# Performance work log

Hardware: AMD Instinct MI355X
Metric: run time of the kernel (lower is better)

## Reference

```python
import jax, jax.numpy as jnp
import numpy as np

P = 16; D = 256; NH = 8; L = 4; E = 8; K = 2; B = 32; IMG = 224; NC = 1000; FF = 4 * D
N = (IMG // P) ** 2  # 196 patches
HD = D // NH  # head dim
EPS = 1e-5


def setup_inputs():
    key = jax.random.key(0)
    ks = iter(jax.random.split(key, 16))
    s = 0.02  # init scale keeps softmax/logits well-conditioned
    rn = lambda shape: jax.random.normal(next(ks), shape, jnp.float32) * s
    return dict(
        x=jax.random.normal(next(ks), (B, 3, IMG, IMG), jnp.float32),
        patch_w=rn((3 * P * P, D)), patch_b=jnp.zeros((D,), jnp.float32),
        cls_token=rn((1, 1, D)), pos_embed=rn((1, N + 1, D)),
        router_w=rn((L, D, E)), router_b=jnp.zeros((L, E), jnp.float32),
        ln1_g=jnp.ones((L, E, D), jnp.float32), ln1_b=jnp.zeros((L, E, D), jnp.float32),
        qkv_w=rn((L, E, D, 3 * D)), qkv_b=jnp.zeros((L, E, 3 * D), jnp.float32),
        proj_w=rn((L, E, D, D)), proj_b=jnp.zeros((L, E, D), jnp.float32),
        ln2_g=jnp.ones((L, E, D), jnp.float32), ln2_b=jnp.zeros((L, E, D), jnp.float32),
        fc1_w=rn((L, E, D, FF)), fc1_b=jnp.zeros((L, E, FF), jnp.float32),
        fc2_w=rn((L, E, FF, D)), fc2_b=jnp.zeros((L, E, D), jnp.float32),
        norm_g=jnp.ones((D,), jnp.float32), norm_b=jnp.zeros((D,), jnp.float32),
        head_w=rn((D, NC)), head_b=jnp.zeros((NC,), jnp.float32),
    )


def _ln(x, g, b):
    m = x.mean(-1, keepdims=True)
    v = ((x - m) ** 2).mean(-1, keepdims=True)
    return (x - m) * jax.lax.rsqrt(v + EPS) * g + b


def _block(x, g1, b1, wqkv, bqkv, wp, bp, g2, b2, w1, bias1, w2, bias2):
    # standard ViT block: LN -> MHA -> residual, LN -> MLP(GELU) -> residual
    bsz, S, _ = x.shape
    h = _ln(x, g1, b1)
    qkv = (h @ wqkv + bqkv).reshape(bsz, S, 3, NH, HD)
    q, k, v = qkv[:, :, 0], qkv[:, :, 1], qkv[:, :, 2]  # [B,S,NH,HD]
    scores = jnp.einsum('bqhd,bkhd->bhqk', q, k) / np.float32(np.sqrt(HD))
    attn = jax.nn.softmax(scores, axis=-1)
    o = jnp.einsum('bhqk,bkhd->bqhd', attn, v).reshape(bsz, S, D)
    x = x + o @ wp + bp
    h2 = _ln(x, g2, b2)
    x = x + jax.nn.gelu(h2 @ w1 + bias1, approximate=False) @ w2 + bias2
    return x


def _moe_layer(x, rw, rb, g1, b1, wqkv, bqkv, wp, bp, g2, b2, w1, bias1, w2, bias2):
    probs = jax.nn.softmax(x @ rw + rb, axis=-1)            # [B,S,E]
    topv, topi = jax.lax.top_k(probs, K)                    # [B,S,K]
    topv = topv / topv.sum(-1, keepdims=True)
    # dense all-expert compute (faithful to source), vmapped over experts
    eo = jax.vmap(_block, in_axes=(None,) + (0,) * 12)(
        x, g1, b1, wqkv, bqkv, wp, bp, g2, b2, w1, bias1, w2, bias2)  # [E,B,S,D]
    eo = jnp.moveaxis(eo, 0, 2)                             # [B,S,E,D]
    sel = jnp.take_along_axis(eo, topi[..., None], axis=2)  # [B,S,K,D]
    return (sel * topv[..., None]).sum(axis=2)


def reference(x, patch_w, patch_b, cls_token, pos_embed, router_w, router_b,
              ln1_g, ln1_b, qkv_w, qkv_b, proj_w, proj_b, ln2_g, ln2_b,
              fc1_w, fc1_b, fc2_w, fc2_b, norm_g, norm_b, head_w, head_b):
    bsz = x.shape[0]
    g = IMG // P
    # patch embed: stride==kernel conv == patch extraction + matmul
    patches = x.reshape(bsz, 3, g, P, g, P).transpose(0, 2, 4, 1, 3, 5).reshape(bsz, N, 3 * P * P)
    h = patches @ patch_w + patch_b                          # [B,N,D]
    cls = jnp.broadcast_to(cls_token, (bsz, 1, D))
    h = jnp.concatenate([cls, h], axis=1) + pos_embed        # [B,N+1,D]
    for l in range(L):
        h = _moe_layer(h, router_w[l], router_b[l], ln1_g[l], ln1_b[l],
                       qkv_w[l], qkv_b[l], proj_w[l], proj_b[l], ln2_g[l], ln2_b[l],
                       fc1_w[l], fc1_b[l], fc2_w[l], fc2_b[l])
    h = _ln(h, norm_g, norm_b)
    return h[:, 0] @ head_w + head_b                         # [B,NC]
```

## Files before the change

### kernel.cpp

```cpp
#include <hip/hip_runtime.h>
#include <math.h>

#define SEQ 197
#define BATCH 32
#define DIM 256
#define NHEAD 8
#define HDIM 32
#define NEXP 8
#define NLAYER 4
#define FFDIM 1024
#define NCLS 1000
#define NPATCH 196
#define TOK (BATCH * SEQ)
#define CAP 13120
#define YB 99
#define YB128 50
#define KT 64

__device__ __forceinline__ void gload16(const float* g, float* l) {
  __builtin_amdgcn_global_load_lds(
      (const __attribute__((address_space(1))) void*)g,
      (__attribute__((address_space(3))) void*)l, 16, 0, 0);
}

__global__ __launch_bounds__(256) void k_im2col(const float* __restrict__ x,
                                                float* __restrict__ Apat) {
  int idx = blockIdx.x * 256 + threadIdx.x;
  if (idx >= BATCH * NPATCH * 768) return;
  int cpp = idx % 768;
  int m = idx / 768;
  int n = m % NPATCH;
  int b = m / NPATCH;
  int c = cpp >> 8;
  int py = (cpp >> 4) & 15;
  int px = cpp & 15;
  int gy = n / 14, gx = n % 14;
  Apat[idx] = x[(((size_t)b * 3 + c) * 224 + gy * 16 + py) * 224 + gx * 16 + px];
}

__global__ __launch_bounds__(256) void k_foldw(const float* __restrict__ qw,
                                               const float* __restrict__ g1,
                                               float* __restrict__ w4) {
  size_t idx = (size_t)blockIdx.x * 256 + threadIdx.x;
  if (idx >= (size_t)32 * 256 * 768) return;
  size_t kn = idx % (256 * 768);
  int le = (int)(idx / (256 * 768));
  int k = (int)(kn / 768);
  w4[idx] = qw[idx] * g1[le * 256 + k];
}

__global__ __launch_bounds__(256) void k_foldb(const float* __restrict__ qw,
                                               const float* __restrict__ qb,
                                               const float* __restrict__ b1,
                                               float* __restrict__ b4) {
  int le = blockIdx.y;
  int col = blockIdx.x * 256 + threadIdx.x;
  const float* w = qw + (size_t)le * 256 * 768 + col;
  const float* lb = b1 + (size_t)le * 256;
  float acc = 0.f;
  for (int k = 0; k < 256; ++k) acc = fmaf(lb[k], w[(size_t)k * 768], acc);
  b4[(size_t)le * 768 + col] = acc + qb[(size_t)le * 768 + col];
}

__global__ __launch_bounds__(256) void k_gemm_t(
    const float* __restrict__ A, const float* __restrict__ W,
    const float* __restrict__ bias, const float* __restrict__ R,
    const float* __restrict__ X2, const float* __restrict__ PW,
    const int* __restrict__ ptok, const int* __restrict__ off_e,
    const int* __restrict__ cnt_e, float* __restrict__ out, int M, int N,
    int K, int Wld, int wcol, int bstride, int ebase, int mode, int flags) {
  __shared__ float As[2][16][68];
  __shared__ float Bs[2][16][128];
  int gx = gridDim.x, gy = gridDim.y;
  int nwg = gx * gy * gridDim.z;
  int lin = blockIdx.x + gx * (blockIdx.y + gy * blockIdx.z);
  int q8 = nwg >> 3, r8 = nwg & 7;
  int xcd = lin & 7, jj0 = lin >> 3;
  int nlin = (xcd < r8 ? xcd * (q8 + 1) : r8 * (q8 + 1) + (xcd - r8) * q8) + jj0;
  int bx = nlin % gx;
  int t1 = nlin / gx;
  int by = t1 % gy;
  int bz = t1 / gy;

  int e = ebase + bz;
  bool seg = (flags & 1) != 0;
  int rows = seg ? cnt_e[e] : M;
  int row0 = by * 64;
  if (row0 >= rows) return;
  int col0 = bx * 128;
  int tid = threadIdx.x;
  int base = seg ? off_e[e] : 0;
  const float* Wp = W + (size_t)e * K * Wld + wcol;
  const float* bp = bias + (size_t)e * bstride + wcol;

  int rr = tid >> 2, kq = (tid & 3) * 4;
  int r = row0 + rr;
  bool val = r < rows;
  int rc = val ? r : rows - 1;
  int gr0 = base + rc;
  int arow = seg ? ((flags & 2) ? ptok[gr0] : gr0) : rc;
  const float* aptr = A + (size_t)arow * K + kq;
  float msk = val ? 1.f : 0.f;
  int wv = tid >> 6, lane = tid & 63;
  const float* bsrc0 =
      Wp + (size_t)(2 * wv + (lane >> 5)) * Wld + col0 + (lane & 31) * 4;
  const float* bsrc1 = bsrc0 + (size_t)8 * Wld;

  gload16(bsrc0, &Bs[0][2 * wv][0]);
  gload16(bsrc1, &Bs[0][8 + 2 * wv][0]);
  {
    float4 av = *(const float4*)aptr;
    As[0][kq + 0][rr] = av.x * msk;
    As[0][kq + 1][rr] = av.y * msk;
    As[0][kq + 2][rr] = av.z * msk;
    As[0][kq + 3][rr] = av.w * msk;
  }
  __syncthreads();

  int tx = tid & 15, ty = tid >> 4;
  float acc0[4][4] = {};
  float acc1[4][4] = {};
  int cur = 0;
  for (int k0 = 0; k0 < K; k0 += 16) {
    int nb = cur ^ 1;
    bool more = (k0 + 16) < K;
    float4 av;
    if (more) {
      av = *(const float4*)(aptr + k0 + 16);
      gload16(bsrc0 + (size_t)(k0 + 16) * Wld, &Bs[nb][2 * wv][0]);
      gload16(bsrc1 + (size_t)(k0 + 16) * Wld, &Bs[nb][8 + 2 * wv][0]);
    }
#pragma unroll
    for (int k = 0; k < 16; ++k) {
      float4 a = *(const float4*)&As[cur][k][ty * 4];
      float4 b0 = *(const float4*)&Bs[cur][k][tx * 4];
      float4 b1 = *(const float4*)&Bs[cur][k][64 + tx * 4];
      float aa[4] = {a.x, a.y, a.z, a.w};
      float b0a[4] = {b0.x, b0.y, b0.z, b0.w};
      float b1a[4] = {b1.x, b1.y, b1.z, b1.w};
#pragma unroll
      for (int i = 0; i < 4; ++i)
#pragma unroll
        for (int j = 0; j < 4; ++j) {
          acc0[i][j] = fmaf(aa[i], b0a[j], acc0[i][j]);
          acc1[i][j] = fmaf(aa[i], b1a[j], acc1[i][j]);
        }
    }
    if (more) {
      As[nb][kq + 0][rr] = av.x * msk;
      As[nb][kq + 1][rr] = av.y * msk;
      As[nb][kq + 2][rr] = av.z * msk;
      As[nb][kq + 3][rr] = av.w * msk;
    }
    __syncthreads();
    cur = nb;
  }
#pragma unroll
  for (int i = 0; i < 4; ++i) {
    int rrow = row0 + ty * 4 + i;
    if (rrow >= rows) continue;
    int gr = base + rrow;
#pragma unroll
    for (int c = 0; c < 2; ++c) {
#pragma unroll
      for (int j = 0; j < 4; ++j) {
        int col = col0 + c * 64 + tx * 4 + j;
        float v = (c ? acc1[i][j] : acc0[i][j]) + bp[col];
        if (mode == 0) {
          size_t orow = seg ? (size_t)gr : (size_t)bz * M + rrow;
          out[orow * N + col] = v;
        } else if (mode == 1) {
          int t = ptok[gr];
          out[(size_t)gr * N + col] = v + R[(size_t)t * N + col];
        } else if (mode == 2) {
          out[(size_t)gr * N + col] =
              0.5f * v * (1.f + erff(v * 0.70710678118654752f));
        } else {
          int t = ptok[gr];
          atomicAdd(&out[(size_t)t * N + col],
                    PW[gr] * (X2[(size_t)gr * N + col] + v));
        }
      }
    }
  }
}

__global__ __launch_bounds__(256) void k_gemm16(
    const float* __restrict__ A, const float* __restrict__ W,
    const float* __restrict__ bias, const float* __restrict__ R,
    const float* __restrict__ X2, const float* __restrict__ PW,
    const int* __restrict__ ptok, const int* __restrict__ off_e,
    const int* __restrict__ cnt_e, float* __restrict__ out, int M, int N,
    int K, int Wld, int wcol, int bstride, int ebase, int mode, int flags) {
  __shared__ float As[2][128][16];
  __shared__ float Bs[2][16][128];
  int gx = gridDim.x, gy = gridDim.y;
  int nwg = gx * gy * gridDim.z;
  int lin = blockIdx.x + gx * (blockIdx.y + gy * blockIdx.z);
  int q8 = nwg >> 3, r8 = nwg & 7;
  int xcd = lin & 7, jj0 = lin >> 3;
  int nlin = (xcd < r8 ? xcd * (q8 + 1) : r8 * (q8 + 1) + (xcd - r8) * q8) + jj0;
  int bx = nlin % gx;
  int t1 = nlin / gx;
  int by = t1 % gy;
  int bz = t1 / gy;

  int e = ebase + bz;
  bool seg = (flags & 1) != 0;
  int rows = seg ? cnt_e[e] : M;
  int row0 = by * 128;
  if (row0 >= rows) return;
  int col0 = bx * 128;
  int tid = threadIdx.x;
  int wv = tid >> 6, lane = tid & 63;
  int base = seg ? off_e[e] : 0;
  const float* Wp = W + (size_t)e * K * Wld + wcol;
  const float* bp = bias + (size_t)e * bstride + wcol;

  const float* pA0;
  const float* pA1;
  {
    int l4 = lane >> 2, lk = (lane & 3) * 4;
#pragma unroll
    for (int c = 0; c < 2; ++c) {
      int r = row0 + wv * 32 + c * 16 + l4;
      int rc = r < rows ? r : rows - 1;
      int gr0 = base + rc;
      int arow = seg ? ((flags & 2) ? ptok[gr0] : gr0) : rc;
      const float* p = A + (size_t)arow * K + lk;
      if (c == 0) pA0 = p; else pA1 = p;
    }
  }
  const float* pB = Wp + (size_t)(4 * wv + (lane >> 5)) * Wld + col0 +
                    (lane & 31) * 4;

  gload16(pA0, &As[0][wv * 32][0]);
  gload16(pA1, &As[0][wv * 32 + 16][0]);
  gload16(pB, &Bs[0][4 * wv][0]);
  gload16(pB + (size_t)2 * Wld, &Bs[0][4 * wv + 2][0]);
  __syncthreads();

  int tx = tid & 15, ty = tid >> 4;
  float acc0[8][4] = {};
  float acc1[8][4] = {};
  int cur = 0;
  for (int k0 = 0; k0 < K; k0 += 16) {
    int nb = cur ^ 1;
    bool more = (k0 + 16) < K;
    if (more) {
      gload16(pA0 + k0 + 16, &As[nb][wv * 32][0]);
      gload16(pA1 + k0 + 16, &As[nb][wv * 32 + 16][0]);
      gload16(pB + (size_t)(k0 + 16) * Wld, &Bs[nb][4 * wv][0]);
      gload16(pB + (size_t)(k0 + 18) * Wld, &Bs[nb][4 * wv + 2][0]);
    }
#pragma unroll
    for (int k4 = 0; k4 < 4; ++k4) {
      float a[8][4];
#pragma unroll
      for (int i = 0; i < 8; ++i) {
        float4 t = *(const float4*)&As[cur][ty + 16 * i][k4 * 4];
        a[i][0] = t.x;
        a[i][1] = t.y;
        a[i][2] = t.z;
        a[i][3] = t.w;
      }
#pragma unroll
      for (int kk = 0; kk < 4; ++kk) {
        float4 b0 = *(const float4*)&Bs[cur][k4 * 4 + kk][tx * 4];
        float4 b1 = *(const float4*)&Bs[cur][k4 * 4 + kk][64 + tx * 4];
        float b0a[4] = {b0.x, b0.y, b0.z, b0.w};
        float b1a[4] = {b1.x, b1.y, b1.z, b1.w};
#pragma unroll
        for (int i = 0; i < 8; ++i) {
          float av = a[i][kk];
#pragma unroll
          for (int j = 0; j < 4; ++j) {
            acc0[i][j] = fmaf(av, b0a[j], acc0[i][j]);
            acc1[i][j] = fmaf(av, b1a[j], acc1[i][j]);
          }
        }
      }
    }
    __syncthreads();
    cur = nb;
  }
#pragma unroll
  for (int i = 0; i < 8; ++i) {
    int rrow = row0 + ty + 16 * i;
    if (rrow >= rows) continue;
    int gr = base + rrow;
#pragma unroll
    for (int c = 0; c < 2; ++c) {
#pragma unroll
      for (int j = 0; j < 4; ++j) {
        int col = col0 + c * 64 + tx * 4 + j;
        float v = (c ? acc1[i][j] : acc0[i][j]) + bp[col];
        if (mode == 0) {
          size_t orow = seg ? (size_t)gr : (size_t)bz * M + rrow;
          out[orow * N + col] = v;
        } else if (mode == 1) {
          int t = ptok[gr];
          out[(size_t)gr * N + col] = v + R[(size_t)t * N + col];
        } else if (mode == 2) {
          out[(size_t)gr * N + col] =
              0.5f * v * (1.f + erff(v * 0.70710678118654752f));
        } else {
          int t = ptok[gr];
          atomicAdd(&out[(size_t)t * N + col],
                    PW[gr] * (X2[(size_t)gr * N + col] + v));
        }
      }
    }
  }
}

__global__ __launch_bounds__(256) void k_assemble(const float* __restrict__ tmp,
                                                  const float* __restrict__ cls,
                                                  const float* __restrict__ pos,
                                                  float* __restrict__ h) {
  int idx = blockIdx.x * 256 + threadIdx.x;
  if (idx >= TOK * DIM) return;
  int d = idx & 255;
  int t = idx >> 8;
  int s = t % SEQ;
  int b = t / SEQ;
  float v = (s == 0) ? cls[d] : tmp[((size_t)b * NPATCH + s - 1) * DIM + d];
  h[idx] = v + pos[s * DIM + d];
}

__global__ __launch_bounds__(64) void k_router(
    const float* __restrict__ h, const float* __restrict__ rw,
    const float* __restrict__ rb, int* __restrict__ cnt_eb,
    int* __restrict__ tmp_s, float* __restrict__ tmp_w) {
  int t = blockIdx.x;
  int lane = threadIdx.x;
  float hv[4];
  const float* hp = h + (size_t)t * DIM + lane * 4;
#pragma unroll
  for (int i = 0; i < 4; i++) hv[i] = hp[i];
  float lg[8];
#pragma unroll
  for (int e = 0; e < 8; e++) {
    float p = 0.f;
#pragma unroll
    for (int i = 0; i < 4; i++) p = fmaf(hv[i], rw[(lane * 4 + i) * 8 + e], p);
#pragma unroll
    for (int off = 32; off; off >>= 1) p += __shfl_down(p, off);
    lg[e] = p;
  }
  if (lane == 0) {
#pragma unroll
    for (int e = 0; e < 8; e++) lg[e] += rb[e];
    float mx = lg[0];
#pragma unroll
    for (int e = 1; e < 8; e++) mx = fmaxf(mx, lg[e]);
    float pr[8];
#pragma unroll
    for (int e = 0; e < 8; e++) pr[e] = expf(lg[e] - mx);
    int i0 = 0;
#pragma unroll
    for (int e = 1; e < 8; e++)
      if (pr[e] > pr[i0]) i0 = e;
    int i1 = -1;
#pragma unroll
    for (int e = 0; e < 8; e++)
      if (e != i0 && (i1 < 0 || pr[e] > pr[i1])) i1 = e;
    float wsum = pr[i0] + pr[i1];
    int b = t / SEQ, s = t - b * SEQ;
    int eb0 = i0 * 32 + b;
    int p0 = atomicAdd(&cnt_eb[eb0], 1);
    tmp_s[eb0 * SEQ + p0] = s;
    tmp_w[eb0 * SEQ + p0] = pr[i0] / wsum;
    int eb1 = i1 * 32 + b;
    int p1 = atomicAdd(&cnt_eb[eb1], 1);
    tmp_s[eb1 * SEQ + p1] = s;
    tmp_w[eb1 * SEQ + p1] = pr[i1] / wsum;
  }
}

__global__ __launch_bounds__(64) void k_scan(const int* __restrict__ cnt_eb,
                                             int* __restrict__ off_eb,
                                             int* __restrict__ off_e,
                                             int* __restrict__ cnt_e) {
  if (threadIdx.x == 0 && blockIdx.x == 0) {
    int g = 0;
    for (int e = 0; e < 8; e++) {
      off_e[e] = g;
      int ce = 0;
      for (int b = 0; b < 32; b++) {
        off_eb[e * 32 + b] = g + ce;
        ce += cnt_eb[e * 32 + b];
      }
      cnt_e[e] = ce;
      g += (ce + 63) & ~63;
    }
  }
}

__global__ __launch_bounds__(256) void k_scatter(
    const int* __restrict__ cnt_eb, const int* __restrict__ off_eb,
    const int* __restrict__ tmp_s, const float* __restrict__ tmp_w,
    int* __restrict__ ptok, float* __restrict__ pw) {
  int eb = blockIdx.x;
  int b = eb & 31;
  int c = cnt_eb[eb];
  int o = off_eb[eb];
  for (int i = threadIdx.x; i < c; i += 256) {
    ptok[o + i] = b * SEQ + tmp_s[eb * SEQ + i];
    pw[o + i] = tmp_w[eb * SEQ + i];
  }
}

__global__ __launch_bounds__(256) void k_ln_noaff(const float* __restrict__ X,
                                                  float* __restrict__ Y) {
  int t = blockIdx.x;
  int d = threadIdx.x;
  float v = X[(size_t)t * DIM + d];
  __shared__ float red[4];
  float s = v;
#pragma unroll
  for (int o = 32; o; o >>= 1) s += __shfl_down(s, o);
  if ((d & 63) == 0) red[d >> 6] = s;
  __syncthreads();
  float mean = (red[0] + red[1] + red[2] + red[3]) * (1.f / 256.f);
  __syncthreads();
  float c = v - mean;
  float s2 = c * c;
#pragma unroll
  for (int o = 32; o; o >>= 1) s2 += __shfl_down(s2, o);
  if ((d & 63) == 0) red[d >> 6] = s2;
  __syncthreads();
  float var = (red[0] + red[1] + red[2] + red[3]) * (1.f / 256.f);
  Y[(size_t)t * DIM + d] = c * rsqrtf(var + 1e-5f);
}

__global__ __launch_bounds__(256) void k_ln_seg(
    const float* __restrict__ X, const float* __restrict__ g,
    const float* __restrict__ bta, float* __restrict__ Y,
    const int* __restrict__ off_e, const int* __restrict__ cnt_e) {
  int e = blockIdx.y;
  int cnt = cnt_e[e];
  int base = off_e[e];
  int d = threadIdx.x;
  float gv = g[e * DIM + d];
  float bv = bta[e * DIM + d];
  __shared__ float red[4];
  for (int r = blockIdx.x; r < cnt; r += gridDim.x) {
    size_t gr = (size_t)(base + r);
    float v = X[gr * DIM + d];
    float s = v;
#pragma unroll
    for (int o = 32; o; o >>= 1) s += __shfl_down(s, o);
    if ((d & 63) == 0) red[d >> 6] = s;
    __syncthreads();
    float mean = (red[0] + red[1] + red[2] + red[3]) * (1.f / 256.f);
    __syncthreads();
    float c = v - mean;
    float s2 = c * c;
#pragma unroll
    for (int o = 32; o; o >>= 1) s2 += __shfl_down(s2, o);
    if ((d & 63) == 0) red[d >> 6] = s2;
    __syncthreads();
    float var = (red[0] + red[1] + red[2] + red[3]) * (1.f / 256.f);
    Y[gr * DIM + d] = c * rsqrtf(var + 1e-5f) * gv + bv;
    __syncthreads();
  }
}

__global__ __launch_bounds__(256) void k_attn(
    const float* __restrict__ qc, const float* __restrict__ kv,
    float* __restrict__ oc, const int* __restrict__ cnt_eb,
    const int* __restrict__ off_eb, int ebase) {
  int bx = blockIdx.x;
  int hh = bx & 7;
  int b = (bx >> 3) & 31;
  int ez = bx >> 8;
  int eb = (ebase + ez) * 32 + b;
  int cnt = cnt_eb[eb];
  if (cnt == 0) return;
  int off = off_eb[eb];
  __shared__ float Ks[KT][HDIM];
  __shared__ float Vs[KT][HDIM];
  const float* base = kv + ((size_t)ez * TOK + (size_t)b * SEQ) * 512;
  int tid = threadIdx.x;
  int grp = tid >> 2;
  int ln = tid & 3;
  int nrounds = (cnt + 63) >> 6;
  for (int qr = 0; qr < nrounds; ++qr) {
    int qi = qr * 64 + grp;
    bool act = qi < cnt;
    int qc_i = act ? qi : cnt - 1;
    const float* qp = qc + (size_t)(off + qc_i) * DIM + hh * HDIM + ln * 8;
    float4 q0 = *(const float4*)qp;
    float4 q1 = *(const float4*)(qp + 4);
    float qv[8] = {q0.x, q0.y, q0.z, q0.w, q1.x, q1.y, q1.z, q1.w};
    float m = -1e30f, l = 0.f;
    float acc[8] = {};
    for (int t0 = 0; t0 < SEQ; t0 += KT) {
      int nk = (SEQ - t0) < KT ? (SEQ - t0) : KT;
      __syncthreads();
      for (int i = tid; i < nk * 16; i += 256) {
        int row = i >> 4, half = (i >> 3) & 1, c4 = (i & 7) * 4;
        const float* p =
            base + (size_t)(t0 + row) * 512 + half * 256 + hh * HDIM + c4;
        if (half == 0)
          *(float4*)&Ks[row][c4] = *(const float4*)p;
        else
          *(float4*)&Vs[row][c4] = *(const float4*)p;
      }
      __syncthreads();
      const float* KsL = &Ks[0][ln * 8];
      const float* VsL = &Vs[0][ln * 8];
#pragma unroll 2
      for (int j = 0; j < nk; ++j) {
        const float4* kr = (const float4*)(KsL + j * HDIM);
        float4 k0 = kr[0], k1 = kr[1];
        float s = qv[0] * k0.x;
        s = fmaf(qv[1], k0.y, s);
        s = fmaf(qv[2], k0.z, s);
        s = fmaf(qv[3], k0.w, s);
        s = fmaf(qv[4], k1.x, s);
        s = fmaf(qv[5], k1.y, s);
        s = fmaf(qv[6], k1.z, s);
        s = fmaf(qv[7], k1.w, s);
        s += __shfl_xor(s, 1);
        s += __shfl_xor(s, 2);
        s *= 0.17677669529663687f;
        float nm = fmaxf(m, s);
        float f = expf(m - nm);
        float e2 = expf(s - nm);
        m = nm;
        l = fmaf(l, f, e2);
        const float4* vr = (const float4*)(VsL + j * HDIM);
        float4 v0 = vr[0], v1 = vr[1];
        acc[0] = fmaf(acc[0], f, e2 * v0.x);
        acc[1] = fmaf(acc[1], f, e2 * v0.y);
        acc[2] = fmaf(acc[2], f, e2 * v0.z);
        acc[3] = fmaf(acc[3], f, e2 * v0.w);
        acc[4] = fmaf(acc[4], f, e2 * v1.x);
        acc[5] = fmaf(acc[5], f, e2 * v1.y);
        acc[6] = fmaf(acc[6], f, e2 * v1.z);
        acc[7] = fmaf(acc[7], f, e2 * v1.w);
      }
    }
    if (act) {
      float inv = 1.f / l;
      float* op = oc + (size_t)(off + qi) * DIM + hh * HDIM + ln * 8;
      float4 o0 = {acc[0] * inv, acc[1] * inv, acc[2] * inv, acc[3] * inv};
      float4 o1 = {acc[4] * inv, acc[5] * inv, acc[6] * inv, acc[7] * inv};
      *(float4*)op = o0;
      *(float4*)(op + 4) = o1;
    }
  }
}

__global__ __launch_bounds__(256) void k_head(const float* __restrict__ h,
                                              const float* __restrict__ ng,
                                              const float* __restrict__ nb,
                                              const float* __restrict__ hw,
                                              const float* __restrict__ hb,
                                              float* __restrict__ out) {
  int b = blockIdx.x;
  int d = threadIdx.x;
  float v = h[(size_t)b * SEQ * DIM + d];
  __shared__ float red[4];
  __shared__ float hls[DIM];
  float s = v;
#pragma unroll
  for (int off = 32; off; off >>= 1) s += __shfl_down(s, off);
  if ((d & 63) == 0) red[d >> 6] = s;
  __syncthreads();
  float mean = (red[0] + red[1] + red[2] + red[3]) * (1.f / 256.f);
  __syncthreads();
  float c = v - mean;
  float s2 = c * c;
#pragma unroll
  for (int off = 32; off; off >>= 1) s2 += __shfl_down(s2, off);
  if ((d & 63) == 0) red[d >> 6] = s2;
  __syncthreads();
  float var = (red[0] + red[1] + red[2] + red[3]) * (1.f / 256.f);
  hls[d] = c * rsqrtf(var + 1e-5f) * ng[d] + nb[d];
  __syncthreads();
  for (int j = d; j < NCLS; j += 256) {
    float sdot = hb[j];
    for (int k2 = 0; k2 < DIM; k2++)
      sdot = fmaf(hls[k2], hw[(size_t)k2 * NCLS + j], sdot);
    out[(size_t)b * NCLS + j] = sdot;
  }
}

extern "C" void kernel_launch(void* const* d_in, const int* in_sizes, int n_in,
                              void* d_out, int out_size, void* d_ws,
                              size_t ws_size, hipStream_t stream) {
  const float* x = (const float*)d_in[0];
  const float* patch_w = (const float*)d_in[1];
  const float* patch_b = (const float*)d_in[2];
  const float* cls_token = (const float*)d_in[3];
  const float* pos_embed = (const float*)d_in[4];
  const float* router_w = (const float*)d_in[5];
  const float* router_b = (const float*)d_in[6];
  const float* ln1_g = (const float*)d_in[7];
  const float* ln1_b = (const float*)d_in[8];
  const float* qkv_w = (const float*)d_in[9];
  const float* qkv_b = (const float*)d_in[10];
  const float* proj_w = (const float*)d_in[11];
  const float* proj_b = (const float*)d_in[12];
  const float* ln2_g = (const float*)d_in[13];
  const float* ln2_b = (const float*)d_in[14];
  const float* fc1_w = (const float*)d_in[15];
  const float* fc1_b = (const float*)d_in[16];
  const float* fc2_w = (const float*)d_in[17];
  const float* fc2_b = (const float*)d_in[18];
  const float* norm_g = (const float*)d_in[19];
  const float* norm_b = (const float*)d_in[20];
  const float* head_w = (const float*)d_in[21];
  const float* head_b = (const float*)d_in[22];

  float* ws = (float*)d_ws;
  size_t off = 0;
  float* xhat = ws + off; off += (size_t)TOK * DIM;
  float* hbuf = ws + off; off += (size_t)TOK * DIM;
  float* accb = ws + off; off += (size_t)TOK * DIM;
  float* qc   = ws + off; off += (size_t)CAP * DIM;
  float* oc   = ws + off; off += (size_t)CAP * DIM;
  float* x2c  = ws + off; off += (size_t)CAP * DIM;
  float* ffc  = ws + off; off += (size_t)CAP * FFDIM;
  float* w4   = ws + off; off += (size_t)32 * DIM * 768;
  float* b4   = ws + off; off += (size_t)32 * 768;
  float* pwb  = ws + off; off += CAP;
  float* tmpw = ws + off; off += 256 * SEQ;
  int* ptok   = (int*)(ws + off); off += CAP;
  int* tmps   = (int*)(ws + off); off += 256 * SEQ;
  int* cnt_eb = (int*)(ws + off); off += 256;
  int* off_eb = (int*)(ws + off); off += 256;
  int* off_e  = (int*)(ws + off); off += 8;
  int* cnt_e  = (int*)(ws + off); off += 8;
  float* kv4 = ffc;
  float* hlnc = qc;

  k_foldw<<<(32 * 256 * 768 + 255) / 256, 256, 0, stream>>>(qkv_w, ln1_g, w4);
  k_foldb<<<dim3(3, 32), 256, 0, stream>>>(qkv_w, qkv_b, ln1_b, b4);

  int tot = BATCH * NPATCH * 768;
  k_im2col<<<(tot + 255) / 256, 256, 0, stream>>>(x, ffc);
  k_gemm16<<<dim3(2, 49, 1), 256, 0, stream>>>(
      ffc, patch_w, patch_b, nullptr, nullptr, nullptr, nullptr, nullptr,
      nullptr, qc, BATCH * NPATCH, DIM, 768, DIM, 0, 0, 0, 0, 0);
  k_assemble<<<(TOK * DIM + 255) / 256, 256, 0, stream>>>(qc, cls_token,
                                                          pos_embed, hbuf);

  float* h = hbuf;
  float* acc = accb;
  for (int l = 0; l < NLAYER; ++l) {
    hipMemsetAsync(acc, 0, (size_t)TOK * DIM * sizeof(float), stream);
    hipMemsetAsync(cnt_eb, 0, 256 * sizeof(int), stream);
    k_router<<<TOK, 64, 0, stream>>>(h, router_w + (size_t)l * DIM * NEXP,
                                     router_b + (size_t)l * NEXP, cnt_eb, tmps,
                                     tmpw);
    k_scan<<<1, 64, 0, stream>>>(cnt_eb, off_eb, off_e, cnt_e);
    k_scatter<<<256, 256, 0, stream>>>(cnt_eb, off_eb, tmps, tmpw, ptok, pwb);
    k_ln_noaff<<<TOK, 256, 0, stream>>>(h, xhat);

    const float* Wl = w4 + (size_t)l * NEXP * DIM * 768;
    const float* Bl = b4 + (size_t)l * NEXP * 768;

    k_gemm_t<<<dim3(2, YB, 8), 256, 0, stream>>>(
        xhat, Wl, Bl, nullptr, nullptr, nullptr, ptok, off_e, cnt_e, qc, 0,
        DIM, DIM, 768, 0, 768, 0, 0, 3);

    for (int grp = 0; grp < 2; ++grp) {
      int eb0 = grp * 4;
      k_gemm16<<<dim3(4, YB128, 4), 256, 0, stream>>>(
          xhat, Wl, Bl, nullptr, nullptr, nullptr, nullptr, nullptr, nullptr,
          kv4, TOK, 512, DIM, 768, 256, 768, eb0, 0, 0);
      k_attn<<<1024, 256, 0, stream>>>(qc, kv4, oc, cnt_eb, off_eb, eb0);
    }

    k_gemm_t<<<dim3(2, YB, 8), 256, 0, stream>>>(
        oc, proj_w + (size_t)l * NEXP * DIM * DIM,
        proj_b + (size_t)l * NEXP * DIM, h, nullptr, nullptr, ptok, off_e,
        cnt_e, x2c, 0, DIM, DIM, DIM, 0, DIM, 0, 1, 1);
    k_ln_seg<<<dim3(YB, 8), 256, 0, stream>>>(
        x2c, ln2_g + (size_t)l * NEXP * DIM, ln2_b + (size_t)l * NEXP * DIM,
        hlnc, off_e, cnt_e);
    k_gemm16<<<dim3(8, YB128, 8), 256, 0, stream>>>(
        hlnc, fc1_w + (size_t)l * NEXP * DIM * FFDIM,
        fc1_b + (size_t)l * NEXP * FFDIM, nullptr, nullptr, nullptr, ptok,
        off_e, cnt_e, ffc, 0, FFDIM, DIM, FFDIM, 0, FFDIM, 0, 2, 1);
    k_gemm_t<<<dim3(2, YB, 8), 256, 0, stream>>>(
        ffc, fc2_w + (size_t)l * NEXP * FFDIM * DIM,
        fc2_b + (size_t)l * NEXP * DIM, nullptr, x2c, pwb, ptok, off_e, cnt_e,
        acc, 0, DIM, FFDIM, DIM, 0, DIM, 0, 3, 1);
    float* t = h;
    h = acc;
    acc = t;
  }
  k_head<<<BATCH, 256, 0, stream>>>(h, norm_g, norm_b, head_w, head_b,
                                    (float*)d_out);
}
```

Before: 3.350 ms.

## Narrow k_gemm_t tiles to 64x64 and add split-K for fc2

The tall GEMM kernel now computes 64x64 output tiles instead of 64x128, which doubles the number of workgroups on the expert QKV-q, proj and fc2 GEMMs. It also gains a split-K mode, used for fc2, where each K-half accumulates through the existing atomicAdd epilogue and only the first split adds bias and residual. The patch-embed GEMM moves from k_gemm16 onto this kernel. The aim is better GPU occupancy for small per-expert GEMMs, at the cost of less register reuse per thread, more redundant A loads, and twice the atomic traffic on fc2.

```diff
diff --git a/kernel.cpp b/kernel.cpp
--- a/kernel.cpp
+++ b/kernel.cpp
@@ -68,9 +68,10 @@
     const float* __restrict__ X2, const float* __restrict__ PW,
     const int* __restrict__ ptok, const int* __restrict__ off_e,
     const int* __restrict__ cnt_e, float* __restrict__ out, int M, int N,
-    int K, int Wld, int wcol, int bstride, int ebase, int mode, int flags) {
+    int K, int Ktot, int ksplit, int Wld, int wcol, int bstride, int ebase,
+    int mode, int flags) {
   __shared__ float As[2][16][68];
-  __shared__ float Bs[2][16][128];
+  __shared__ float Bs[2][16][64];
   int gx = gridDim.x, gy = gridDim.y;
   int nwg = gx * gy * gridDim.z;
   int lin = blockIdx.x + gx * (blockIdx.y + gy * blockIdx.z);
@@ -80,17 +81,21 @@
   int bx = nlin % gx;
   int t1 = nlin / gx;
   int by = t1 % gy;
-  int bz = t1 / gy;
-
-  int e = ebase + bz;
+  int bzf = t1 / gy;
+  int kz = bzf % ksplit;
+  int ez = bzf / ksplit;
+
+  int e = ebase + ez;
   bool seg = (flags & 1) != 0;
+  bool first = (kz == 0);
   int rows = seg ? cnt_e[e] : M;
   int row0 = by * 64;
   if (row0 >= rows) return;
-  int col0 = bx * 128;
+  int col0 = bx * 64;
+  int kbase = kz * K;
   int tid = threadIdx.x;
   int base = seg ? off_e[e] : 0;
-  const float* Wp = W + (size_t)e * K * Wld + wcol;
+  const float* Wp = W + (size_t)e * Ktot * Wld + wcol;
   const float* bp = bias + (size_t)e * bstride + wcol;
 
   int rr = tid >> 2, kq = (tid & 3) * 4;
@@ -99,15 +104,13 @@
   int rc = val ? r : rows - 1;
   int gr0 = base + rc;
   int arow = seg ? ((flags & 2) ? ptok[gr0] : gr0) : rc;
-  const float* aptr = A + (size_t)arow * K + kq;
+  const float* aptr = A + (size_t)arow * Ktot + kbase + kq;
   float msk = val ? 1.f : 0.f;
   int wv = tid >> 6, lane = tid & 63;
-  const float* bsrc0 =
-      Wp + (size_t)(2 * wv + (lane >> 5)) * Wld + col0 + (lane & 31) * 4;
-  const float* bsrc1 = bsrc0 + (size_t)8 * Wld;
-
-  gload16(bsrc0, &Bs[0][2 * wv][0]);
-  gload16(bsrc1, &Bs[0][8 + 2 * wv][0]);
+  const float* bsrc = Wp + (size_t)(kbase + 4 * wv + (lane >> 4)) * Wld +
+                      col0 + (lane & 15) * 4;
+
+  gload16(bsrc, &Bs[0][4 * wv][0]);
   {
     float4 av = *(const float4*)aptr;
     As[0][kq + 0][rr] = av.x * msk;
@@ -118,8 +121,7 @@
   __syncthreads();
 
   int tx = tid & 15, ty = tid >> 4;
-  float acc0[4][4] = {};
-  float acc1[4][4] = {};
+  float acc[4][4] = {};
   int cur = 0;
   for (int k0 = 0; k0 < K; k0 += 16) {
     int nb = cur ^ 1;
@@ -127,24 +129,18 @@
     float4 av;
     if (more) {
       av = *(const float4*)(aptr + k0 + 16);
-      gload16(bsrc0 + (size_t)(k0 + 16) * Wld, &Bs[nb][2 * wv][0]);
-      gload16(bsrc1 + (size_t)(k0 + 16) * Wld, &Bs[nb][8 + 2 * wv][0]);
+      gload16(bsrc + (size_t)(k0 + 16) * Wld, &Bs[nb][4 * wv][0]);
     }
 #pragma unroll
     for (int k = 0; k < 16; ++k) {
       float4 a = *(const float4*)&As[cur][k][ty * 4];
-      float4 b0 = *(const float4*)&Bs[cur][k][tx * 4];
-      float4 b1 = *(const float4*)&Bs[cur][k][64 + tx * 4];
+      float4 b = *(const float4*)&Bs[cur][k][tx * 4];
       float aa[4] = {a.x, a.y, a.z, a.w};
-      float b0a[4] = {b0.x, b0.y, b0.z, b0.w};
-      float b1a[4] = {b1.x, b1.y, b1.z, b1.w};
+      float bb[4] = {b.x, b.y, b.z, b.w};
 #pragma unroll
       for (int i = 0; i < 4; ++i)
 #pragma unroll
-        for (int j = 0; j < 4; ++j) {
-          acc0[i][j] = fmaf(aa[i], b0a[j], acc0[i][j]);
-          acc1[i][j] = fmaf(aa[i], b1a[j], acc1[i][j]);
-        }
+        for (int j = 0; j < 4; ++j) acc[i][j] = fmaf(aa[i], bb[j], acc[i][j]);
     }
     if (more) {
       As[nb][kq + 0][rr] = av.x * msk;
@@ -161,25 +157,22 @@
     if (rrow >= rows) continue;
     int gr = base + rrow;
 #pragma unroll
-    for (int c = 0; c < 2; ++c) {
-#pragma unroll
-      for (int j = 0; j < 4; ++j) {
-        int col = col0 + c * 64 + tx * 4 + j;
-        float v = (c ? acc1[i][j] : acc0[i][j]) + bp[col];
-        if (mode == 0) {
-          size_t orow = seg ? (size_t)gr : (size_t)bz * M + rrow;
-          out[orow * N + col] = v;
-        } else if (mode == 1) {
-          int t = ptok[gr];
-          out[(size_t)gr * N + col] = v + R[(size_t)t * N + col];
-        } else if (mode == 2) {
-          out[(size_t)gr * N + col] =
-              0.5f * v * (1.f + erff(v * 0.70710678118654752f));
-        } else {
-          int t = ptok[gr];
-          atomicAdd(&out[(size_t)t * N + col],
-                    PW[gr] * (X2[(size_t)gr * N + col] + v));
-        }
+    for (int j = 0; j < 4; ++j) {
+      int col = col0 + tx * 4 + j;
+      float v = acc[i][j] + (first ? bp[col] : 0.f);
+      if (mode == 0) {
+        size_t orow = seg ? (size_t)gr : (size_t)bzf * M + rrow;
+        out[orow * N + col] = v;
+      } else if (mode == 1) {
+        int t = ptok[gr];
+        out[(size_t)gr * N + col] = v + R[(size_t)t * N + col];
+      } else if (mode == 2) {
+        out[(size_t)gr * N + col] =
+            0.5f * v * (1.f + erff(v * 0.70710678118654752f));
+      } else {
+        int t = ptok[gr];
+        float x2v = first ? X2[(size_t)gr * N + col] : 0.f;
+        atomicAdd(&out[(size_t)t * N + col], PW[gr] * (x2v + v));
       }
     }
   }
@@ -643,9 +636,9 @@
 
   int tot = BATCH * NPATCH * 768;
   k_im2col<<<(tot + 255) / 256, 256, 0, stream>>>(x, ffc);
-  k_gemm16<<<dim3(2, 49, 1), 256, 0, stream>>>(
+  k_gemm_t<<<dim3(4, 98, 1), 256, 0, stream>>>(
       ffc, patch_w, patch_b, nullptr, nullptr, nullptr, nullptr, nullptr,
-      nullptr, qc, BATCH * NPATCH, DIM, 768, DIM, 0, 0, 0, 0, 0);
+      nullptr, qc, BATCH * NPATCH, DIM, 768, 768, 1, DIM, 0, 0, 0, 0, 0);
   k_assemble<<<(TOK * DIM + 255) / 256, 256, 0, stream>>>(qc, cls_token,
                                                           pos_embed, hbuf);
 
@@ -664,9 +657,9 @@
     const float* Wl = w4 + (size_t)l * NEXP * DIM * 768;
     const float* Bl = b4 + (size_t)l * NEXP * 768;
 
-    k_gemm_t<<<dim3(2, YB, 8), 256, 0, stream>>>(
+    k_gemm_t<<<dim3(4, YB, 8), 256, 0, stream>>>(
         xhat, Wl, Bl, nullptr, nullptr, nullptr, ptok, off_e, cnt_e, qc, 0,
-        DIM, DIM, 768, 0, 768, 0, 0, 3);
+        DIM, DIM, DIM, 1, 768, 0, 768, 0, 0, 3);
 
     for (int grp = 0; grp < 2; ++grp) {
       int eb0 = grp * 4;
@@ -676,10 +669,10 @@
       k_attn<<<1024, 256, 0, stream>>>(qc, kv4, oc, cnt_eb, off_eb, eb0);
     }
 
-    k_gemm_t<<<dim3(2, YB, 8), 256, 0, stream>>>(
+    k_gemm_t<<<dim3(4, YB, 8), 256, 0, stream>>>(
         oc, proj_w + (size_t)l * NEXP * DIM * DIM,
         proj_b + (size_t)l * NEXP * DIM, h, nullptr, nullptr, ptok, off_e,
-        cnt_e, x2c, 0, DIM, DIM, DIM, 0, DIM, 0, 1, 1);
+        cnt_e, x2c, 0, DIM, DIM, DIM, 1, DIM, 0, DIM, 0, 1, 1);
     k_ln_seg<<<dim3(YB, 8), 256, 0, stream>>>(
         x2c, ln2_g + (size_t)l * NEXP * DIM, ln2_b + (size_t)l * NEXP * DIM,
         hlnc, off_e, cnt_e);
@@ -687,10 +680,10 @@
         hlnc, fc1_w + (size_t)l * NEXP * DIM * FFDIM,
         fc1_b + (size_t)l * NEXP * FFDIM, nullptr, nullptr, nullptr, ptok,
         off_e, cnt_e, ffc, 0, FFDIM, DIM, FFDIM, 0, FFDIM, 0, 2, 1);
-    k_gemm_t<<<dim3(2, YB, 8), 256, 0, stream>>>(
+    k_gemm_t<<<dim3(4, YB, 16), 256, 0, stream>>>(
         ffc, fc2_w + (size_t)l * NEXP * FFDIM * DIM,
         fc2_b + (size_t)l * NEXP * DIM, nullptr, x2c, pwb, ptok, off_e, cnt_e,
-        acc, 0, DIM, FFDIM, DIM, 0, DIM, 0, 3, 1);
+        acc, 0, DIM, 512, FFDIM, 2, DIM, 0, DIM, 0, 3, 1);
     float* t = h;
     h = acc;
     acc = t;
```

Result: slower. 3.464 ms (+3.4%).

## Load GEMM A tiles directly to LDS row-major and reuse k_gemm_t for patch embed

Applied to the files above, without the earlier changes.

The A tile in k_gemm_t is now fetched with async global-to-LDS 16-byte loads into a row-major [64][16] layout, replacing register-staged transposed stores. The inner loop is restructured to read four A rows per k-quad from LDS. The patch-embedding GEMM switches from k_gemm16 to k_gemm_t with a doubled row grid. The intent is to remove the VGPR round trip and the strided LDS writes on A. The cost is that out-of-range rows are no longer zero-masked (they load a clamped valid row and rely on output skipping), and the new row-major As reads may cause LDS bank conflicts.

```diff
diff --git a/kernel.cpp b/kernel.cpp
--- a/kernel.cpp
+++ b/kernel.cpp
@@ -69,7 +69,7 @@
     const int* __restrict__ ptok, const int* __restrict__ off_e,
     const int* __restrict__ cnt_e, float* __restrict__ out, int M, int N,
     int K, int Wld, int wcol, int bstride, int ebase, int mode, int flags) {
-  __shared__ float As[2][16][68];
+  __shared__ float As[2][64][16];
   __shared__ float Bs[2][16][128];
   int gx = gridDim.x, gy = gridDim.y;
   int nwg = gx * gy * gridDim.z;
@@ -89,32 +89,26 @@
   if (row0 >= rows) return;
   int col0 = bx * 128;
   int tid = threadIdx.x;
+  int wv = tid >> 6, lane = tid & 63;
   int base = seg ? off_e[e] : 0;
   const float* Wp = W + (size_t)e * K * Wld + wcol;
   const float* bp = bias + (size_t)e * bstride + wcol;
 
-  int rr = tid >> 2, kq = (tid & 3) * 4;
-  int r = row0 + rr;
-  bool val = r < rows;
-  int rc = val ? r : rows - 1;
-  int gr0 = base + rc;
-  int arow = seg ? ((flags & 2) ? ptok[gr0] : gr0) : rc;
-  const float* aptr = A + (size_t)arow * K + kq;
-  float msk = val ? 1.f : 0.f;
-  int wv = tid >> 6, lane = tid & 63;
+  const float* pA;
+  {
+    int r = row0 + wv * 16 + (lane >> 2);
+    int rc = r < rows ? r : rows - 1;
+    int gr0 = base + rc;
+    int arow = seg ? ((flags & 2) ? ptok[gr0] : gr0) : rc;
+    pA = A + (size_t)arow * K + (lane & 3) * 4;
+  }
   const float* bsrc0 =
       Wp + (size_t)(2 * wv + (lane >> 5)) * Wld + col0 + (lane & 31) * 4;
   const float* bsrc1 = bsrc0 + (size_t)8 * Wld;
 
+  gload16(pA, &As[0][wv * 16][0]);
   gload16(bsrc0, &Bs[0][2 * wv][0]);
   gload16(bsrc1, &Bs[0][8 + 2 * wv][0]);
-  {
-    float4 av = *(const float4*)aptr;
-    As[0][kq + 0][rr] = av.x * msk;
-    As[0][kq + 1][rr] = av.y * msk;
-    As[0][kq + 2][rr] = av.z * msk;
-    As[0][kq + 3][rr] = av.w * msk;
-  }
   __syncthreads();
 
   int tx = tid & 15, ty = tid >> 4;
@@ -124,33 +118,38 @@
   for (int k0 = 0; k0 < K; k0 += 16) {
     int nb = cur ^ 1;
     bool more = (k0 + 16) < K;
-    float4 av;
     if (more) {
-      av = *(const float4*)(aptr + k0 + 16);
+      gload16(pA + k0 + 16, &As[nb][wv * 16][0]);
       gload16(bsrc0 + (size_t)(k0 + 16) * Wld, &Bs[nb][2 * wv][0]);
       gload16(bsrc1 + (size_t)(k0 + 16) * Wld, &Bs[nb][8 + 2 * wv][0]);
     }
 #pragma unroll
-    for (int k = 0; k < 16; ++k) {
-      float4 a = *(const float4*)&As[cur][k][ty * 4];
-      float4 b0 = *(const float4*)&Bs[cur][k][tx * 4];
-      float4 b1 = *(const float4*)&Bs[cur][k][64 + tx * 4];
-      float aa[4] = {a.x, a.y, a.z, a.w};
-      float b0a[4] = {b0.x, b0.y, b0.z, b0.w};
-      float b1a[4] = {b1.x, b1.y, b1.z, b1.w};
-#pragma unroll
-      for (int i = 0; i < 4; ++i)
-#pragma unroll
-        for (int j = 0; j < 4; ++j) {
-          acc0[i][j] = fmaf(aa[i], b0a[j], acc0[i][j]);
-          acc1[i][j] = fmaf(aa[i], b1a[j], acc1[i][j]);
+    for (int k4 = 0; k4 < 4; ++k4) {
+      float a[4][4];
+#pragma unroll
+      for (int i = 0; i < 4; ++i) {
+        float4 t = *(const float4*)&As[cur][ty * 4 + i][k4 * 4];
+        a[i][0] = t.x;
+        a[i][1] = t.y;
+        a[i][2] = t.z;
+        a[i][3] = t.w;
+      }
+#pragma unroll
+      for (int kk = 0; kk < 4; ++kk) {
+        float4 b0 = *(const float4*)&Bs[cur][k4 * 4 + kk][tx * 4];
+        float4 b1 = *(const float4*)&Bs[cur][k4 * 4 + kk][64 + tx * 4];
+        float b0a[4] = {b0.x, b0.y, b0.z, b0.w};
+        float b1a[4] = {b1.x, b1.y, b1.z, b1.w};
+#pragma unroll
+        for (int i = 0; i < 4; ++i) {
+          float av = a[i][kk];
+#pragma unroll
+          for (int j = 0; j < 4; ++j) {
+            acc0[i][j] = fmaf(av, b0a[j], acc0[i][j]);
+            acc1[i][j] = fmaf(av, b1a[j], acc1[i][j]);
+          }
         }
-    }
-    if (more) {
-      As[nb][kq + 0][rr] = av.x * msk;
-      As[nb][kq + 1][rr] = av.y * msk;
-      As[nb][kq + 2][rr] = av.z * msk;
-      As[nb][kq + 3][rr] = av.w * msk;
+      }
     }
     __syncthreads();
     cur = nb;
@@ -643,7 +642,7 @@
 
   int tot = BATCH * NPATCH * 768;
   k_im2col<<<(tot + 255) / 256, 256, 0, stream>>>(x, ffc);
-  k_gemm16<<<dim3(2, 49, 1), 256, 0, stream>>>(
+  k_gemm_t<<<dim3(2, 98, 1), 256, 0, stream>>>(
       ffc, patch_w, patch_b, nullptr, nullptr, nullptr, nullptr, nullptr,
       nullptr, qc, BATCH * NPATCH, DIM, 768, DIM, 0, 0, 0, 0, 0);
   k_assemble<<<(TOK * DIM + 255) / 256, 256, 0, stream>>>(qc, cls_token,
```

Measured after the change: 3.381 ms. About the same (+0.9%).
